# Performance work log

Measured on AMD Instinct MI355X. Metric: run time of the kernel, lower is better.

Reference implementation:

```python
import jax, jax.numpy as jnp
import numpy as np
from jax.experimental.ode import odeint

IN, H, OUT, NLAYERS = 256, 512, 128, 5
BATCH = 1024
RTOL, ATOL = 1e-7, 1e-9  # torchdiffeq dopri5 defaults


def _lin_init(key, fan_in, fan_out):
    kw, kb = jax.random.split(key)
    s = 1.0 / np.sqrt(fan_in)
    W = jax.random.uniform(kw, (fan_in, fan_out), jnp.float32, -s, s)
    b = jax.random.uniform(kb, (fan_out,), jnp.float32, -s, s)
    return W, b


def setup_inputs() -> dict:
    key = jax.random.key(0)
    ks = jax.random.split(key, 32)
    x = jax.random.normal(ks[0], (BATCH, IN), jnp.float32)
    Wi1, bi1 = _lin_init(ks[1], IN, H)
    Wi2, bi2 = _lin_init(ks[2], H, H)
    Wr, br = _lin_init(ks[3], IN, H)
    # 5 ODE funcs: Linear(H,2H) Tanh Linear(2H,2H) Tanh Linear(2H,H)
    oW1, ob1, oW2, ob2, oW3, ob3 = [], [], [], [], [], []
    for i in range(NLAYERS):
        a, b_ = _lin_init(ks[4 + 3 * i], H, 2 * H)
        c, d = _lin_init(ks[5 + 3 * i], 2 * H, 2 * H)
        e, f = _lin_init(ks[6 + 3 * i], 2 * H, H)
        oW1.append(a); ob1.append(b_); oW2.append(c); ob2.append(d); oW3.append(e); ob3.append(f)
    Wo1, bo1 = _lin_init(ks[20], H, H)
    Wo2, bo2 = _lin_init(ks[21], H, OUT)
    return {
        "x": x,
        "Wi1": Wi1, "bi1": bi1, "Wi2": Wi2, "bi2": bi2,
        "Wr": Wr, "br": br,
        "ode_W1": jnp.stack(oW1), "ode_b1": jnp.stack(ob1),
        "ode_W2": jnp.stack(oW2), "ode_b2": jnp.stack(ob2),
        "ode_W3": jnp.stack(oW3), "ode_b3": jnp.stack(ob3),
        "Wo1": Wo1, "bo1": bo1, "Wo2": Wo2, "bo2": bo2,
    }


def _forward(x, Wi1, bi1, Wi2, bi2, Wr, br,
             ode_W1, ode_b1, ode_W2, ode_b2, ode_W3, ode_b3,
             Wo1, bo1, Wo2, bo2):
    t = jnp.linspace(0.0, 1.0, 10)
    residual = x @ Wr + br                                  # [B, H]
    h = jnp.tanh(jnp.tanh(x @ Wi1 + bi1) @ Wi2 + bi2) + residual
    for i in range(NLAYERS):
        W1, b1 = ode_W1[i], ode_b1[i]
        W2, b2 = ode_W2[i], ode_b2[i]
        W3, b3 = ode_W3[i], ode_b3[i]

        def f(y, t_, W1=W1, b1=b1, W2=W2, b2=b2, W3=W3, b3=b3):
            return jnp.tanh(jnp.tanh(y @ W1 + b1) @ W2 + b2) @ W3 + b3

        h = odeint(f, h, t, rtol=RTOL, atol=ATOL)[-1]       # dopri5, take t=1
    return jnp.tanh(jnp.tanh(h @ Wo1 + bo1) @ Wo2 + bo2)   # [B, OUT]


def reference(x, Wi1, bi1, Wi2, bi2, Wr, br,
              ode_W1, ode_b1, ode_W2, ode_b2, ode_W3, ode_b3,
              Wo1, bo1, Wo2, bo2):
    return _forward(x, Wi1, bi1, Wi2, bi2, Wr, br,
                    ode_W1, ode_b1, ode_W2, ode_b2, ode_W3, ode_b3,
                    Wo1, bo1, Wo2, bo2)
```

## Files before the change

kernel.cpp:

```cpp
#include <hip/hip_runtime.h>
#include <hip/hip_bf16.h>
#include <math.h>

#define BATCH 1024
#define RKSTEPS 16

typedef __bf16 bf16x8 __attribute__((ext_vector_type(8)));
typedef float f32x16 __attribute__((ext_vector_type(16)));

enum { EM_PLAIN_F32=0, EM_TANH=1, EM_TANH_RES=2, EM_RK_FIRST=3, EM_RK_MID=4, EM_RK_LAST=5, EM_TANH_OUT=6 };

__device__ __forceinline__ unsigned short f2bf(float f){
    unsigned int u = __float_as_uint(f);
    u += 0x7fffu + ((u >> 16) & 1u);
    return (unsigned short)(u >> 16);
}
__device__ __forceinline__ float bf2f(unsigned short h){
    return __uint_as_float(((unsigned int)h) << 16);
}

__global__ __launch_bounds__(256) void xsplit(const float* __restrict__ src,
                                              unsigned short* __restrict__ h,
                                              unsigned short* __restrict__ l, int n){
    int i = blockIdx.x * 256 + threadIdx.x;
    if (i < n){
        float v = src[i];
        unsigned short hh = f2bf(v);
        h[i] = hh;
        l[i] = f2bf(v - bf2f(hh));
    }
}

__global__ __launch_bounds__(256) void wsplit_t(const float* __restrict__ W,
                                                unsigned short* __restrict__ Th,
                                                unsigned short* __restrict__ Tl,
                                                int K, int N){
    __shared__ float tile[32][33];
    const int k0 = blockIdx.x * 32;
    const int n0 = blockIdx.y * 32;
    const int t = threadIdx.x;
    const int r = t >> 3;
    const int c4 = (t & 7) * 4;
    const float4 v = *(const float4*)&W[(size_t)(k0 + r) * N + n0 + c4];
    tile[r][c4+0] = v.x; tile[r][c4+1] = v.y; tile[r][c4+2] = v.z; tile[r][c4+3] = v.w;
    __syncthreads();
    ushort4 hh, ll;
    #pragma unroll
    for (int j = 0; j < 4; ++j){
        float x = tile[c4 + j][r];
        unsigned short hb = f2bf(x);
        ((unsigned short*)&hh)[j] = hb;
        ((unsigned short*)&ll)[j] = f2bf(x - bf2f(hb));
    }
    *(ushort4*)&Th[(size_t)(n0 + r) * K + k0 + c4] = hh;
    *(ushort4*)&Tl[(size_t)(n0 + r) * K + k0 + c4] = ll;
}

__global__ __launch_bounds__(128) void gemm3p(
    const unsigned short* __restrict__ Ah, const unsigned short* __restrict__ Al,
    const unsigned short* __restrict__ Bh, const unsigned short* __restrict__ Bl,
    const float* __restrict__ bias,
    int M, int N, int K, int mode, float wk, float hc,
    unsigned short* __restrict__ outh, unsigned short* __restrict__ outl,
    float* outf, const float* res32, float* kacc32)
{
    __shared__ unsigned short Ash[32][72];
    __shared__ unsigned short Asl[32][72];
    __shared__ unsigned short Bsh[64][72];
    __shared__ unsigned short Bsl[64][72];

    const int tid  = threadIdx.x;
    const int lane = tid & 63;
    const int w    = tid >> 6;
    const int m0   = blockIdx.y * 32;
    const int n0   = blockIdx.x * 64;

    f32x16 accA, accB;
    #pragma unroll
    for (int i = 0; i < 16; ++i){ accA[i] = 0.f; accB[i] = 0.f; }

    uint4 rAh[2], rAl[2], rBh[4], rBl[4];

    auto stage_load = [&](int k0){
        #pragma unroll
        for (int p = 0; p < 2; ++p){
            int id = p * 128 + tid; int r = id >> 3; int c = (id & 7) * 8;
            size_t off = (size_t)(m0 + r) * K + k0 + c;
            rAh[p] = *(const uint4*)&Ah[off];
            rAl[p] = *(const uint4*)&Al[off];
        }
        #pragma unroll
        for (int p = 0; p < 4; ++p){
            int id = p * 128 + tid; int r = id >> 3; int c = (id & 7) * 8;
            size_t off = (size_t)(n0 + r) * K + k0 + c;
            rBh[p] = *(const uint4*)&Bh[off];
            rBl[p] = *(const uint4*)&Bl[off];
        }
    };
    auto stage_write = [&](){
        #pragma unroll
        for (int p = 0; p < 2; ++p){
            int id = p * 128 + tid; int r = id >> 3; int c = (id & 7) * 8;
            *(uint4*)&Ash[r][c] = rAh[p];
            *(uint4*)&Asl[r][c] = rAl[p];
        }
        #pragma unroll
        for (int p = 0; p < 4; ++p){
            int id = p * 128 + tid; int r = id >> 3; int c = (id & 7) * 8;
            *(uint4*)&Bsh[r][c] = rBh[p];
            *(uint4*)&Bsl[r][c] = rBl[p];
        }
    };

    stage_load(0);
    stage_write();
    __syncthreads();

    const int arow = lane & 31;
    const int brow = w * 32 + (lane & 31);
    const int g8   = (lane >> 5) * 8;

    for (int k0 = 0; k0 < K; k0 += 64){
        const bool more = (k0 + 64) < K;
        if (more) stage_load(k0 + 64);
        #pragma unroll
        for (int kc = 0; kc < 4; ++kc){
            const int koff = kc * 16 + g8;
            bf16x8 a_h = *(const bf16x8*)&Ash[arow][koff];
            bf16x8 a_l = *(const bf16x8*)&Asl[arow][koff];
            bf16x8 b_h = *(const bf16x8*)&Bsh[brow][koff];
            bf16x8 b_l = *(const bf16x8*)&Bsl[brow][koff];
            accA = __builtin_amdgcn_mfma_f32_32x32x16_bf16(a_h, b_h, accA, 0, 0, 0);
            accB = __builtin_amdgcn_mfma_f32_32x32x16_bf16(a_h, b_l, accB, 0, 0, 0);
            accB = __builtin_amdgcn_mfma_f32_32x32x16_bf16(a_l, b_h, accB, 0, 0, 0);
        }
        if (more){
            __syncthreads();
            stage_write();
            __syncthreads();
        }
    }

    const int col = n0 + w * 32 + (lane & 31);
    const float bc = bias[col];
    const int g4 = (lane >> 5) * 4;
    #pragma unroll
    for (int r = 0; r < 16; ++r){
        const int row = m0 + (r & 3) + 8 * (r >> 2) + g4;
        const size_t idx = (size_t)row * N + col;
        float z = accA[r] + accB[r] + bc;
        if (mode == EM_PLAIN_F32){
            outf[idx] = z;
        } else if (mode == EM_TANH){
            float t = tanhf(z);
            unsigned short hh = f2bf(t);
            outh[idx] = hh; outl[idx] = f2bf(t - bf2f(hh));
        } else if (mode == EM_TANH_RES){
            float t = tanhf(z) + res32[idx];
            outf[idx] = t;
            unsigned short hh = f2bf(t);
            outh[idx] = hh; outl[idx] = f2bf(t - bf2f(hh));
        } else if (mode == EM_RK_FIRST){
            kacc32[idx] = z;
            float yt = res32[idx] + hc * z;
            unsigned short hh = f2bf(yt);
            outh[idx] = hh; outl[idx] = f2bf(yt - bf2f(hh));
        } else if (mode == EM_RK_MID){
            kacc32[idx] += wk * z;
            float yt = res32[idx] + hc * z;
            unsigned short hh = f2bf(yt);
            outh[idx] = hh; outl[idx] = f2bf(yt - bf2f(hh));
        } else if (mode == EM_RK_LAST){
            float ynew = res32[idx] + hc * (kacc32[idx] + z);
            outf[idx] = ynew;
            unsigned short hh = f2bf(ynew);
            outh[idx] = hh; outl[idx] = f2bf(ynew - bf2f(hh));
        } else {
            outf[idx] = tanhf(z);
        }
    }
}

extern "C" void kernel_launch(void* const* d_in, const int* in_sizes, int n_in,
                              void* d_out, int out_size, void* d_ws, size_t ws_size,
                              hipStream_t stream)
{
    (void)in_sizes; (void)n_in; (void)out_size; (void)ws_size;
    const float* x   = (const float*)d_in[0];
    const float* Wi1 = (const float*)d_in[1];
    const float* bi1 = (const float*)d_in[2];
    const float* Wi2 = (const float*)d_in[3];
    const float* bi2 = (const float*)d_in[4];
    const float* Wr  = (const float*)d_in[5];
    const float* br  = (const float*)d_in[6];
    const float* oW1 = (const float*)d_in[7];
    const float* ob1 = (const float*)d_in[8];
    const float* oW2 = (const float*)d_in[9];
    const float* ob2 = (const float*)d_in[10];
    const float* oW3 = (const float*)d_in[11];
    const float* ob3 = (const float*)d_in[12];
    const float* Wo1 = (const float*)d_in[13];
    const float* bo1 = (const float*)d_in[14];
    const float* Wo2 = (const float*)d_in[15];
    const float* bo2 = (const float*)d_in[16];
    float* out = (float*)d_out;

    typedef unsigned short us;
    char* p = (char*)d_ws;
    auto alloc = [&](size_t bytes)->char*{ char* r = p; p += (bytes + 255) & ~(size_t)255; return r; };

    us* xh = (us*)alloc(1024*256*2);  us* xl = (us*)alloc(1024*256*2);
    us* Wi1th = (us*)alloc(512*256*2);  us* Wi1tl = (us*)alloc(512*256*2);
    us* Wi2th = (us*)alloc(512*512*2);  us* Wi2tl = (us*)alloc(512*512*2);
    us* Wrth  = (us*)alloc(512*256*2);  us* Wrtl  = (us*)alloc(512*256*2);
    us* oW1th = (us*)alloc(5ull*1024*512*2);  us* oW1tl = (us*)alloc(5ull*1024*512*2);
    us* oW2th = (us*)alloc(5ull*1024*1024*2); us* oW2tl = (us*)alloc(5ull*1024*1024*2);
    us* oW3th = (us*)alloc(5ull*512*1024*2);  us* oW3tl = (us*)alloc(5ull*512*1024*2);
    us* Wo1th = (us*)alloc(512*512*2);  us* Wo1tl = (us*)alloc(512*512*2);
    us* Wo2th = (us*)alloc(128*512*2);  us* Wo2tl = (us*)alloc(128*512*2);
    us* t1h = (us*)alloc(1024ull*1024*2); us* t1l = (us*)alloc(1024ull*1024*2);
    us* a2h = (us*)alloc(1024ull*1024*2); us* a2l = (us*)alloc(1024ull*1024*2);
    us* yh  = (us*)alloc(1024ull*512*2);  us* yl  = (us*)alloc(1024ull*512*2);
    us* yth = (us*)alloc(1024ull*512*2);  us* ytl = (us*)alloc(1024ull*512*2);
    float* y32  = (float*)alloc(1024ull*512*4);
    float* kacc = (float*)alloc(1024ull*512*4);
    float* rres = (float*)alloc(1024ull*512*4);

    hipLaunchKernelGGL(xsplit, dim3(1024), dim3(256), 0, stream, x, xh, xl, 1024*256);
    auto WS = [&](const float* W, us* th, us* tl, int K, int N){
        hipLaunchKernelGGL(wsplit_t, dim3(K/32, N/32), dim3(256), 0, stream, W, th, tl, K, N);
    };
    WS(Wi1, Wi1th, Wi1tl, 256, 512);
    WS(Wi2, Wi2th, Wi2tl, 512, 512);
    WS(Wr,  Wrth,  Wrtl,  256, 512);
    for (int L = 0; L < 5; ++L){
        WS(oW1 + (size_t)L*512*1024,  oW1th + (size_t)L*1024*512,  oW1tl + (size_t)L*1024*512,  512, 1024);
        WS(oW2 + (size_t)L*1024*1024, oW2th + (size_t)L*1024*1024, oW2tl + (size_t)L*1024*1024, 1024, 1024);
        WS(oW3 + (size_t)L*1024*512,  oW3th + (size_t)L*512*1024,  oW3tl + (size_t)L*512*1024,  1024, 512);
    }
    WS(Wo1, Wo1th, Wo1tl, 512, 512);
    WS(Wo2, Wo2th, Wo2tl, 512, 128);

    auto G = [&](const us* ah, const us* al, const us* bh, const us* bl,
                 const float* bias, int N, int K, int mode, float wkv, float hcv,
                 us* oh, us* ol, float* of, const float* rs, float* ka){
        dim3 grid(N/64, BATCH/32);
        hipLaunchKernelGGL(gemm3p, grid, dim3(128), 0, stream,
                           ah, al, bh, bl, bias, BATCH, N, K, mode, wkv, hcv, oh, ol, of, rs, ka);
    };

    G(xh, xl, Wrth, Wrtl, br, 512, 256, EM_PLAIN_F32, 0.f, 0.f, nullptr, nullptr, rres, nullptr, nullptr);
    G(xh, xl, Wi1th, Wi1tl, bi1, 512, 256, EM_TANH, 0.f, 0.f, t1h, t1l, nullptr, nullptr, nullptr);
    G(t1h, t1l, Wi2th, Wi2tl, bi2, 512, 512, EM_TANH_RES, 0.f, 0.f, yh, yl, y32, rres, nullptr);

    const float hs = 1.0f / (float)RKSTEPS;
    for (int L = 0; L < 5; ++L){
        const us* W1h = oW1th + (size_t)L*1024*512;  const us* W1l = oW1tl + (size_t)L*1024*512;
        const us* W2h = oW2th + (size_t)L*1024*1024; const us* W2l = oW2tl + (size_t)L*1024*1024;
        const us* W3h = oW3th + (size_t)L*512*1024;  const us* W3l = oW3tl + (size_t)L*512*1024;
        const float* b1 = ob1 + (size_t)L*1024;
        const float* b2 = ob2 + (size_t)L*1024;
        const float* b3 = ob3 + (size_t)L*512;
        for (int s = 0; s < RKSTEPS; ++s){
            G(yh, yl, W1h, W1l, b1, 1024, 512,  EM_TANH, 0.f, 0.f, t1h, t1l, nullptr, nullptr, nullptr);
            G(t1h, t1l, W2h, W2l, b2, 1024, 1024, EM_TANH, 0.f, 0.f, a2h, a2l, nullptr, nullptr, nullptr);
            G(a2h, a2l, W3h, W3l, b3, 512, 1024, EM_RK_FIRST, 0.f, 0.5f*hs, yth, ytl, nullptr, y32, kacc);
            G(yth, ytl, W1h, W1l, b1, 1024, 512,  EM_TANH, 0.f, 0.f, t1h, t1l, nullptr, nullptr, nullptr);
            G(t1h, t1l, W2h, W2l, b2, 1024, 1024, EM_TANH, 0.f, 0.f, a2h, a2l, nullptr, nullptr, nullptr);
            G(a2h, a2l, W3h, W3l, b3, 512, 1024, EM_RK_MID, 2.f, 0.5f*hs, yth, ytl, nullptr, y32, kacc);
            G(yth, ytl, W1h, W1l, b1, 1024, 512,  EM_TANH, 0.f, 0.f, t1h, t1l, nullptr, nullptr, nullptr);
            G(t1h, t1l, W2h, W2l, b2, 1024, 1024, EM_TANH, 0.f, 0.f, a2h, a2l, nullptr, nullptr, nullptr);
            G(a2h, a2l, W3h, W3l, b3, 512, 1024, EM_RK_MID, 2.f, hs, yth, ytl, nullptr, y32, kacc);
            G(yth, ytl, W1h, W1l, b1, 1024, 512,  EM_TANH, 0.f, 0.f, t1h, t1l, nullptr, nullptr, nullptr);
            G(t1h, t1l, W2h, W2l, b2, 1024, 1024, EM_TANH, 0.f, 0.f, a2h, a2l, nullptr, nullptr, nullptr);
            G(a2h, a2l, W3h, W3l, b3, 512, 1024, EM_RK_LAST, 1.f, hs/6.f, yh, yl, y32, y32, kacc);
        }
    }

    G(yh, yl, Wo1th, Wo1tl, bo1, 512, 512, EM_TANH, 0.f, 0.f, t1h, t1l, nullptr, nullptr, nullptr);
    G(t1h, t1l, Wo2th, Wo2tl, bo2, 128, 512, EM_TANH_OUT, 0.f, 0.f, nullptr, nullptr, out, nullptr, nullptr);
}
```

Measured before the change: 43.26 ms.

## Fuse ODE RK4 loop into persistent kernel with grid barriers

Replaces the 960 separate GEMM launches of the RK4 integration with one persistent kernel of 256 blocks that loops over layers, steps and stages. A software grid barrier built on an atomic counter separates the GEMM phases. All 22 weight-split launches are merged into one table-driven kernel. This removes per-launch overhead and tail gaps, but it relies on all 256 blocks being co-resident, uses a timeout break in the barrier, and the third GEMM leaves half of its waves idle.

```diff
diff --git a/kernel.cpp b/kernel.cpp
--- a/kernel.cpp
+++ b/kernel.cpp
@@ -4,70 +4,83 @@
 
 #define BATCH 1024
 #define RKSTEPS 16
-
+#define NBLK 256
+
+typedef unsigned short us;
 typedef __bf16 bf16x8 __attribute__((ext_vector_type(8)));
 typedef float f32x16 __attribute__((ext_vector_type(16)));
 
-enum { EM_PLAIN_F32=0, EM_TANH=1, EM_TANH_RES=2, EM_RK_FIRST=3, EM_RK_MID=4, EM_RK_LAST=5, EM_TANH_OUT=6 };
-
-__device__ __forceinline__ unsigned short f2bf(float f){
+enum { EM_PLAIN_F32=0, EM_TANH=1, EM_TANH_RES=2, EM_TANH_OUT=6 };
+
+__device__ __forceinline__ us f2bf(float f){
     unsigned int u = __float_as_uint(f);
     u += 0x7fffu + ((u >> 16) & 1u);
-    return (unsigned short)(u >> 16);
-}
-__device__ __forceinline__ float bf2f(unsigned short h){
+    return (us)(u >> 16);
+}
+__device__ __forceinline__ float bf2f(us h){
     return __uint_as_float(((unsigned int)h) << 16);
 }
+__device__ __forceinline__ void split_store(float v, us* ph, us* pl, size_t idx){
+    us hh = f2bf(v); ph[idx] = hh; pl[idx] = f2bf(v - bf2f(hh));
+}
 
 __global__ __launch_bounds__(256) void xsplit(const float* __restrict__ src,
-                                              unsigned short* __restrict__ h,
-                                              unsigned short* __restrict__ l, int n){
+                                              us* __restrict__ h, us* __restrict__ l,
+                                              int n, unsigned* ctr){
+    if (blockIdx.x == 0 && threadIdx.x == 0) *ctr = 0u;
     int i = blockIdx.x * 256 + threadIdx.x;
     if (i < n){
         float v = src[i];
-        unsigned short hh = f2bf(v);
+        us hh = f2bf(v);
         h[i] = hh;
         l[i] = f2bf(v - bf2f(hh));
     }
 }
 
-__global__ __launch_bounds__(256) void wsplit_t(const float* __restrict__ W,
-                                                unsigned short* __restrict__ Th,
-                                                unsigned short* __restrict__ Tl,
-                                                int K, int N){
+struct WsDesc { const float* src; us* h; us* l; int K; int N; int tile0; };
+struct WsTable { WsDesc d[22]; };
+
+__global__ __launch_bounds__(256) void wsplit_all(WsTable T){
     __shared__ float tile[32][33];
-    const int k0 = blockIdx.x * 32;
-    const int n0 = blockIdx.y * 32;
-    const int t = threadIdx.x;
-    const int r = t >> 3;
-    const int c4 = (t & 7) * 4;
-    const float4 v = *(const float4*)&W[(size_t)(k0 + r) * N + n0 + c4];
+    const int t = blockIdx.x;
+    int mi = 0;
+    #pragma unroll 1
+    for (int i = 1; i < 22; ++i) if (t >= T.d[i].tile0) mi = i;
+    const WsDesc dd = T.d[mi];
+    const int local = t - dd.tile0;
+    const int tilesx = dd.K >> 5;
+    const int k0 = (local % tilesx) * 32;
+    const int n0 = (local / tilesx) * 32;
+    const int tt = threadIdx.x;
+    const int r = tt >> 3;
+    const int c4 = (tt & 7) * 4;
+    const float4 v = *(const float4*)&dd.src[(size_t)(k0 + r) * dd.N + n0 + c4];
     tile[r][c4+0] = v.x; tile[r][c4+1] = v.y; tile[r][c4+2] = v.z; tile[r][c4+3] = v.w;
     __syncthreads();
     ushort4 hh, ll;
     #pragma unroll
     for (int j = 0; j < 4; ++j){
         float x = tile[c4 + j][r];
-        unsigned short hb = f2bf(x);
-        ((unsigned short*)&hh)[j] = hb;
-        ((unsigned short*)&ll)[j] = f2bf(x - bf2f(hb));
-    }
-    *(ushort4*)&Th[(size_t)(n0 + r) * K + k0 + c4] = hh;
-    *(ushort4*)&Tl[(size_t)(n0 + r) * K + k0 + c4] = ll;
+        us hb = f2bf(x);
+        ((us*)&hh)[j] = hb;
+        ((us*)&ll)[j] = f2bf(x - bf2f(hb));
+    }
+    *(ushort4*)&dd.h[(size_t)(n0 + r) * dd.K + k0 + c4] = hh;
+    *(ushort4*)&dd.l[(size_t)(n0 + r) * dd.K + k0 + c4] = ll;
 }
 
 __global__ __launch_bounds__(128) void gemm3p(
-    const unsigned short* __restrict__ Ah, const unsigned short* __restrict__ Al,
-    const unsigned short* __restrict__ Bh, const unsigned short* __restrict__ Bl,
+    const us* __restrict__ Ah, const us* __restrict__ Al,
+    const us* __restrict__ Bh, const us* __restrict__ Bl,
     const float* __restrict__ bias,
-    int M, int N, int K, int mode, float wk, float hc,
-    unsigned short* __restrict__ outh, unsigned short* __restrict__ outl,
-    float* outf, const float* res32, float* kacc32)
+    int M, int N, int K, int mode,
+    us* __restrict__ outh, us* __restrict__ outl,
+    float* outf, const float* res32)
 {
-    __shared__ unsigned short Ash[32][72];
-    __shared__ unsigned short Asl[32][72];
-    __shared__ unsigned short Bsh[64][72];
-    __shared__ unsigned short Bsl[64][72];
+    __shared__ us Ash[32][72];
+    __shared__ us Asl[32][72];
+    __shared__ us Bsh[64][72];
+    __shared__ us Bsl[64][72];
 
     const int tid  = threadIdx.x;
     const int lane = tid & 63;
@@ -80,7 +93,6 @@
     for (int i = 0; i < 16; ++i){ accA[i] = 0.f; accB[i] = 0.f; }
 
     uint4 rAh[2], rAl[2], rBh[4], rBl[4];
-
     auto stage_load = [&](int k0){
         #pragma unroll
         for (int p = 0; p < 2; ++p){
@@ -153,30 +165,247 @@
             outf[idx] = z;
         } else if (mode == EM_TANH){
             float t = tanhf(z);
-            unsigned short hh = f2bf(t);
-            outh[idx] = hh; outl[idx] = f2bf(t - bf2f(hh));
+            split_store(t, outh, outl, idx);
         } else if (mode == EM_TANH_RES){
             float t = tanhf(z) + res32[idx];
             outf[idx] = t;
-            unsigned short hh = f2bf(t);
-            outh[idx] = hh; outl[idx] = f2bf(t - bf2f(hh));
-        } else if (mode == EM_RK_FIRST){
-            kacc32[idx] = z;
-            float yt = res32[idx] + hc * z;
-            unsigned short hh = f2bf(yt);
-            outh[idx] = hh; outl[idx] = f2bf(yt - bf2f(hh));
-        } else if (mode == EM_RK_MID){
-            kacc32[idx] += wk * z;
-            float yt = res32[idx] + hc * z;
-            unsigned short hh = f2bf(yt);
-            outh[idx] = hh; outl[idx] = f2bf(yt - bf2f(hh));
-        } else if (mode == EM_RK_LAST){
-            float ynew = res32[idx] + hc * (kacc32[idx] + z);
-            outf[idx] = ynew;
-            unsigned short hh = f2bf(ynew);
-            outh[idx] = hh; outl[idx] = f2bf(ynew - bf2f(hh));
+            split_store(t, outh, outl, idx);
         } else {
             outf[idx] = tanhf(z);
+        }
+    }
+}
+
+__device__ __forceinline__ void grid_bar(unsigned* ctr, unsigned target){
+    __syncthreads();
+    if (threadIdx.x == 0){
+        __threadfence();
+        __hip_atomic_fetch_add(ctr, 1u, __ATOMIC_ACQ_REL, __HIP_MEMORY_SCOPE_AGENT);
+        long long t0 = (long long)__builtin_amdgcn_s_memrealtime();
+        while (__hip_atomic_load(ctr, __ATOMIC_ACQUIRE, __HIP_MEMORY_SCOPE_AGENT) < target){
+            __builtin_amdgcn_s_sleep(1);
+            if ((long long)__builtin_amdgcn_s_memrealtime() - t0 > 200000000LL) break;
+        }
+        __threadfence();
+    }
+    __syncthreads();
+}
+
+__global__ __launch_bounds__(256, 1) void fused_ode(
+    const us* __restrict__ W1t_h, const us* __restrict__ W1t_l, const float* __restrict__ B1,
+    const us* __restrict__ W2t_h, const us* __restrict__ W2t_l, const float* __restrict__ B2,
+    const us* __restrict__ W3t_h, const us* __restrict__ W3t_l, const float* __restrict__ B3,
+    us* __restrict__ yh,  us* __restrict__ yl,
+    us* __restrict__ yth, us* __restrict__ ytl,
+    us* __restrict__ a1h, us* __restrict__ a1l,
+    us* __restrict__ a2h, us* __restrict__ a2l,
+    float* __restrict__ y32, float* __restrict__ kacc,
+    unsigned* ctr)
+{
+    __shared__ us smem[18432];
+    us* Ash = smem;
+    us* Asl = smem + 4608;
+    us* Bsh = smem + 9216;
+    us* Bsl = smem + 13824;
+
+    const int tid  = threadIdx.x;
+    const int lane = tid & 63;
+    const int w    = tid >> 6;
+    const int bid  = blockIdx.x;
+    const int mrow = (bid & 7) * 2 + ((bid >> 3) & 1);
+    const int ncol = bid >> 4;
+    const int m0  = mrow * 64;
+    const int n0  = ncol * 64;
+    const int n0c = ncol * 32;
+    const float hs = 1.0f / (float)RKSTEPS;
+    unsigned epoch = 0;
+
+    auto gemm64 = [&](const us* Ahp, const us* Alp, int sA,
+                      const us* Bhp, const us* Blp, int K,
+                      f32x16& c0, f32x16& c1, f32x16& c2){
+        uint4 rAh[2], rAl[2], rBh[2], rBl[2];
+        auto ld = [&](int k0){
+            #pragma unroll
+            for (int p = 0; p < 2; ++p){
+                int id = p * 256 + tid; int rr = id >> 3; int cc = (id & 7) * 8;
+                rAh[p] = *(const uint4*)&Ahp[(size_t)rr * sA + k0 + cc];
+                rAl[p] = *(const uint4*)&Alp[(size_t)rr * sA + k0 + cc];
+                rBh[p] = *(const uint4*)&Bhp[(size_t)rr * K + k0 + cc];
+                rBl[p] = *(const uint4*)&Blp[(size_t)rr * K + k0 + cc];
+            }
+        };
+        auto wr = [&](){
+            #pragma unroll
+            for (int p = 0; p < 2; ++p){
+                int id = p * 256 + tid; int rr = id >> 3; int cc = (id & 7) * 8;
+                *(uint4*)&Ash[rr * 72 + cc] = rAh[p];
+                *(uint4*)&Asl[rr * 72 + cc] = rAl[p];
+                *(uint4*)&Bsh[rr * 72 + cc] = rBh[p];
+                *(uint4*)&Bsl[rr * 72 + cc] = rBl[p];
+            }
+        };
+        const int aoff = ((w >> 1) * 32 + (lane & 31)) * 72;
+        const int boff = ((w & 1)  * 32 + (lane & 31)) * 72;
+        const int g8   = (lane >> 5) * 8;
+        ld(0);
+        for (int k0 = 0; k0 < K; k0 += 64){
+            wr(); __syncthreads();
+            if (k0 + 64 < K) ld(k0 + 64);
+            #pragma unroll
+            for (int kc = 0; kc < 4; ++kc){
+                int ko = kc * 16 + g8;
+                bf16x8 ah = *(const bf16x8*)&Ash[aoff + ko];
+                bf16x8 al = *(const bf16x8*)&Asl[aoff + ko];
+                bf16x8 bh = *(const bf16x8*)&Bsh[boff + ko];
+                bf16x8 bl = *(const bf16x8*)&Bsl[boff + ko];
+                c0 = __builtin_amdgcn_mfma_f32_32x32x16_bf16(ah, bh, c0, 0, 0, 0);
+                c1 = __builtin_amdgcn_mfma_f32_32x32x16_bf16(ah, bl, c1, 0, 0, 0);
+                c2 = __builtin_amdgcn_mfma_f32_32x32x16_bf16(al, bh, c2, 0, 0, 0);
+            }
+            __syncthreads();
+        }
+    };
+
+    auto gemmC = [&](const us* Ahp, const us* Alp,
+                     const us* Bhp, const us* Blp,
+                     f32x16& c0, f32x16& c1, f32x16& c2){
+        uint4 rAh[2], rAl[2], rBh, rBl;
+        auto ld = [&](int k0){
+            #pragma unroll
+            for (int p = 0; p < 2; ++p){
+                int id = p * 256 + tid; int rr = id >> 3; int cc = (id & 7) * 8;
+                rAh[p] = *(const uint4*)&Ahp[(size_t)rr * 1024 + k0 + cc];
+                rAl[p] = *(const uint4*)&Alp[(size_t)rr * 1024 + k0 + cc];
+            }
+            { int rr = tid >> 3; int cc = (tid & 7) * 8;
+              rBh = *(const uint4*)&Bhp[(size_t)rr * 1024 + k0 + cc];
+              rBl = *(const uint4*)&Blp[(size_t)rr * 1024 + k0 + cc]; }
+        };
+        auto wr = [&](){
+            #pragma unroll
+            for (int p = 0; p < 2; ++p){
+                int id = p * 256 + tid; int rr = id >> 3; int cc = (id & 7) * 8;
+                *(uint4*)&Ash[rr * 72 + cc] = rAh[p];
+                *(uint4*)&Asl[rr * 72 + cc] = rAl[p];
+            }
+            { int rr = tid >> 3; int cc = (tid & 7) * 8;
+              *(uint4*)&Bsh[rr * 72 + cc] = rBh;
+              *(uint4*)&Bsl[rr * 72 + cc] = rBl; }
+        };
+        const int aoff = ((w & 1) * 32 + (lane & 31)) * 72;
+        const int boff = (lane & 31) * 72;
+        const int g8   = (lane >> 5) * 8;
+        ld(0);
+        for (int k0 = 0; k0 < 1024; k0 += 64){
+            wr(); __syncthreads();
+            if (k0 + 64 < 1024) ld(k0 + 64);
+            if (w < 2){
+                #pragma unroll
+                for (int kc = 0; kc < 4; ++kc){
+                    int ko = kc * 16 + g8;
+                    bf16x8 ah = *(const bf16x8*)&Ash[aoff + ko];
+                    bf16x8 al = *(const bf16x8*)&Asl[aoff + ko];
+                    bf16x8 bh = *(const bf16x8*)&Bsh[boff + ko];
+                    bf16x8 bl = *(const bf16x8*)&Bsl[boff + ko];
+                    c0 = __builtin_amdgcn_mfma_f32_32x32x16_bf16(ah, bh, c0, 0, 0, 0);
+                    c1 = __builtin_amdgcn_mfma_f32_32x32x16_bf16(ah, bl, c1, 0, 0, 0);
+                    c2 = __builtin_amdgcn_mfma_f32_32x32x16_bf16(al, bh, c2, 0, 0, 0);
+                }
+            }
+            __syncthreads();
+        }
+    };
+
+    #pragma unroll 1
+    for (int L = 0; L < 5; ++L){
+        const us* W1h = W1t_h + (size_t)L * 1024 * 512;
+        const us* W1l = W1t_l + (size_t)L * 1024 * 512;
+        const us* W2h = W2t_h + (size_t)L * 1024 * 1024;
+        const us* W2l = W2t_l + (size_t)L * 1024 * 1024;
+        const us* W3h = W3t_h + (size_t)L * 512 * 1024;
+        const us* W3l = W3t_l + (size_t)L * 512 * 1024;
+        const float* b1 = B1 + L * 1024;
+        const float* b2 = B2 + L * 1024;
+        const float* b3 = B3 + L * 512;
+
+        #pragma unroll 1
+        for (int st = 0; st < RKSTEPS; ++st){
+            #pragma unroll 1
+            for (int s = 0; s < 4; ++s){
+                const us* inh = (s == 0) ? yh : yth;
+                const us* inl = (s == 0) ? yl : ytl;
+
+                {
+                    f32x16 c0, c1, c2;
+                    #pragma unroll
+                    for (int i = 0; i < 16; ++i){ c0[i]=0.f; c1[i]=0.f; c2[i]=0.f; }
+                    gemm64(inh + (size_t)m0 * 512, inl + (size_t)m0 * 512, 512,
+                           W1h + (size_t)n0 * 512, W1l + (size_t)n0 * 512, 512,
+                           c0, c1, c2);
+                    const int col = n0 + (w & 1) * 32 + (lane & 31);
+                    const float bb = b1[col];
+                    const int rbase = m0 + (w >> 1) * 32 + 4 * (lane >> 5);
+                    #pragma unroll
+                    for (int r = 0; r < 16; ++r){
+                        int row = rbase + (r & 3) + 8 * (r >> 2);
+                        float z = c0[r] + c1[r] + c2[r] + bb;
+                        split_store(tanhf(z), a1h, a1l, (size_t)row * 1024 + col);
+                    }
+                }
+                ++epoch; grid_bar(ctr, epoch * NBLK);
+
+                {
+                    f32x16 c0, c1, c2;
+                    #pragma unroll
+                    for (int i = 0; i < 16; ++i){ c0[i]=0.f; c1[i]=0.f; c2[i]=0.f; }
+                    gemm64(a1h + (size_t)m0 * 1024, a1l + (size_t)m0 * 1024, 1024,
+                           W2h + (size_t)n0 * 1024, W2l + (size_t)n0 * 1024, 1024,
+                           c0, c1, c2);
+                    const int col = n0 + (w & 1) * 32 + (lane & 31);
+                    const float bb = b2[col];
+                    const int rbase = m0 + (w >> 1) * 32 + 4 * (lane >> 5);
+                    #pragma unroll
+                    for (int r = 0; r < 16; ++r){
+                        int row = rbase + (r & 3) + 8 * (r >> 2);
+                        float z = c0[r] + c1[r] + c2[r] + bb;
+                        split_store(tanhf(z), a2h, a2l, (size_t)row * 1024 + col);
+                    }
+                }
+                ++epoch; grid_bar(ctr, epoch * NBLK);
+
+                {
+                    f32x16 c0, c1, c2;
+                    #pragma unroll
+                    for (int i = 0; i < 16; ++i){ c0[i]=0.f; c1[i]=0.f; c2[i]=0.f; }
+                    gemmC(a2h + (size_t)m0 * 1024, a2l + (size_t)m0 * 1024,
+                          W3h + (size_t)n0c * 1024, W3l + (size_t)n0c * 1024,
+                          c0, c1, c2);
+                    if (w < 2){
+                        const int col = n0c + (lane & 31);
+                        const float bb = b3[col];
+                        const int rbase = m0 + (w & 1) * 32 + 4 * (lane >> 5);
+                        #pragma unroll
+                        for (int r = 0; r < 16; ++r){
+                            int row = rbase + (r & 3) + 8 * (r >> 2);
+                            size_t idx = (size_t)row * 512 + col;
+                            float z = c0[r] + c1[r] + c2[r] + bb;
+                            if (s == 0){
+                                kacc[idx] = z;
+                                split_store(y32[idx] + 0.5f * hs * z, yth, ytl, idx);
+                            } else if (s == 3){
+                                float yn = y32[idx] + (hs / 6.0f) * (kacc[idx] + z);
+                                y32[idx] = yn;
+                                split_store(yn, yh, yl, idx);
+                            } else {
+                                kacc[idx] += 2.0f * z;
+                                float hc = (s == 1) ? 0.5f * hs : hs;
+                                split_store(y32[idx] + hc * z, yth, ytl, idx);
+                            }
+                        }
+                    }
+                }
+                ++epoch; grid_bar(ctr, epoch * NBLK);
+            }
         }
     }
 }
@@ -205,7 +434,6 @@
     const float* bo2 = (const float*)d_in[16];
     float* out = (float*)d_out;
 
-    typedef unsigned short us;
     char* p = (char*)d_ws;
     auto alloc = [&](size_t bytes)->char*{ char* r = p; p += (bytes + 255) & ~(size_t)255; return r; };
 
@@ -218,65 +446,57 @@
     us* oW3th = (us*)alloc(5ull*512*1024*2);  us* oW3tl = (us*)alloc(5ull*512*1024*2);
     us* Wo1th = (us*)alloc(512*512*2);  us* Wo1tl = (us*)alloc(512*512*2);
     us* Wo2th = (us*)alloc(128*512*2);  us* Wo2tl = (us*)alloc(128*512*2);
-    us* t1h = (us*)alloc(1024ull*1024*2); us* t1l = (us*)alloc(1024ull*1024*2);
+    us* t1h = (us*)alloc(1024ull*512*2);  us* t1l = (us*)alloc(1024ull*512*2);
+    us* a1h = (us*)alloc(1024ull*1024*2); us* a1l = (us*)alloc(1024ull*1024*2);
     us* a2h = (us*)alloc(1024ull*1024*2); us* a2l = (us*)alloc(1024ull*1024*2);
     us* yh  = (us*)alloc(1024ull*512*2);  us* yl  = (us*)alloc(1024ull*512*2);
     us* yth = (us*)alloc(1024ull*512*2);  us* ytl = (us*)alloc(1024ull*512*2);
     float* y32  = (float*)alloc(1024ull*512*4);
     float* kacc = (float*)alloc(1024ull*512*4);
-    float* rres = (float*)alloc(1024ull*512*4);
-
-    hipLaunchKernelGGL(xsplit, dim3(1024), dim3(256), 0, stream, x, xh, xl, 1024*256);
-    auto WS = [&](const float* W, us* th, us* tl, int K, int N){
-        hipLaunchKernelGGL(wsplit_t, dim3(K/32, N/32), dim3(256), 0, stream, W, th, tl, K, N);
+    unsigned* ctr = (unsigned*)alloc(256);
+    float* rres = kacc;
+
+    hipLaunchKernelGGL(xsplit, dim3(1024), dim3(256), 0, stream, x, xh, xl, 1024*256, ctr);
+
+    WsTable T;
+    for (int i = 0; i < 22; ++i){
+        T.d[i].src = nullptr; T.d[i].h = nullptr; T.d[i].l = nullptr;
+        T.d[i].K = 32; T.d[i].N = 32; T.d[i].tile0 = 0x7fffffff;
+    }
+    int tile_acc = 0, di = 0;
+    auto addW = [&](const float* W, us* th, us* tl, int K, int N){
+        T.d[di].src = W; T.d[di].h = th; T.d[di].l = tl;
+        T.d[di].K = K; T.d[di].N = N; T.d[di].tile0 = tile_acc;
+        tile_acc += (K/32) * (N/32); ++di;
     };
-    WS(Wi1, Wi1th, Wi1tl, 256, 512);
-    WS(Wi2, Wi2th, Wi2tl, 512, 512);
-    WS(Wr,  Wrth,  Wrtl,  256, 512);
+    addW(Wi1, Wi1th, Wi1tl, 256, 512);
+    addW(Wi2, Wi2th, Wi2tl, 512, 512);
+    addW(Wr,  Wrth,  Wrtl,  256, 512);
     for (int L = 0; L < 5; ++L){
-        WS(oW1 + (size_t)L*512*1024,  oW1th + (size_t)L*1024*512,  oW1tl + (size_t)L*1024*512,  512, 1024);
-        WS(oW2 + (size_t)L*1024*1024, oW2th + (size_t)L*1024*1024, oW2tl + (size_t)L*1024*1024, 1024, 1024);
-        WS(oW3 + (size_t)L*1024*512,  oW3th + (size_t)L*512*1024,  oW3tl + (size_t)L*512*1024,  1024, 512);
-    }
-    WS(Wo1, Wo1th, Wo1tl, 512, 512);
-    WS(Wo2, Wo2th, Wo2tl, 512, 128);
+        addW(oW1 + (size_t)L*512*1024,  oW1th + (size_t)L*1024*512,  oW1tl + (size_t)L*1024*512,  512, 1024);
+        addW(oW2 + (size_t)L*1024*1024, oW2th + (size_t)L*1024*1024, oW2tl + (size_t)L*1024*1024, 1024, 1024);
+        addW(oW3 + (size_t)L*1024*512,  oW3th + (size_t)L*512*1024,  oW3tl + (size_t)L*512*1024,  1024, 512);
+    }
+    addW(Wo1, Wo1th, Wo1tl, 512, 512);
+    addW(Wo2, Wo2th, Wo2tl, 512, 128);
+    hipLaunchKernelGGL(wsplit_all, dim3(tile_acc), dim3(256), 0, stream, T);
 
     auto G = [&](const us* ah, const us* al, const us* bh, const us* bl,
-                 const float* bias, int N, int K, int mode, float wkv, float hcv,
-                 us* oh, us* ol, float* of, const float* rs, float* ka){
+                 const float* bias, int N, int K, int mode,
+                 us* oh, us* ol, float* of, const float* rs){
         dim3 grid(N/64, BATCH/32);
         hipLaunchKernelGGL(gemm3p, grid, dim3(128), 0, stream,
-                           ah, al, bh, bl, bias, BATCH, N, K, mode, wkv, hcv, oh, ol, of, rs, ka);
+                           ah, al, bh, bl, bias, BATCH, N, K, mode, oh, ol, of, rs);
     };
 
-    G(xh, xl, Wrth, Wrtl, br, 512, 256, EM_PLAIN_F32, 0.f, 0.f, nullptr, nullptr, rres, nullptr, nullptr);
-    G(xh, xl, Wi1th, Wi1tl, bi1, 512, 256, EM_TANH, 0.f, 0.f, t1h, t1l, nullptr, nullptr, nullptr);
-    G(t1h, t1l, Wi2th, Wi2tl, bi2, 512, 512, EM_TANH_RES, 0.f, 0.f, yh, yl, y32, rres, nullptr);
-
-    const float hs = 1.0f / (float)RKSTEPS;
-    for (int L = 0; L < 5; ++L){
-        const us* W1h = oW1th + (size_t)L*1024*512;  const us* W1l = oW1tl + (size_t)L*1024*512;
-        const us* W2h = oW2th + (size_t)L*1024*1024; const us* W2l = oW2tl + (size_t)L*1024*1024;
-        const us* W3h = oW3th + (size_t)L*512*1024;  const us* W3l = oW3tl + (size_t)L*512*1024;
-        const float* b1 = ob1 + (size_t)L*1024;
-        const float* b2 = ob2 + (size_t)L*1024;
-        const float* b3 = ob3 + (size_t)L*512;
-        for (int s = 0; s < RKSTEPS; ++s){
-            G(yh, yl, W1h, W1l, b1, 1024, 512,  EM_TANH, 0.f, 0.f, t1h, t1l, nullptr, nullptr, nullptr);
-            G(t1h, t1l, W2h, W2l, b2, 1024, 1024, EM_TANH, 0.f, 0.f, a2h, a2l, nullptr, nullptr, nullptr);
-            G(a2h, a2l, W3h, W3l, b3, 512, 1024, EM_RK_FIRST, 0.f, 0.5f*hs, yth, ytl, nullptr, y32, kacc);
-            G(yth, ytl, W1h, W1l, b1, 1024, 512,  EM_TANH, 0.f, 0.f, t1h, t1l, nullptr, nullptr, nullptr);
-            G(t1h, t1l, W2h, W2l, b2, 1024, 1024, EM_TANH, 0.f, 0.f, a2h, a2l, nullptr, nullptr, nullptr);
-            G(a2h, a2l, W3h, W3l, b3, 512, 1024, EM_RK_MID, 2.f, 0.5f*hs, yth, ytl, nullptr, y32, kacc);
-            G(yth, ytl, W1h, W1l, b1, 1024, 512,  EM_TANH, 0.f, 0.f, t1h, t1l, nullptr, nullptr, nullptr);
-            G(t1h, t1l, W2h, W2l, b2, 1024, 1024, EM_TANH, 0.f, 0.f, a2h, a2l, nullptr, nullptr, nullptr);
-            G(a2h, a2l, W3h, W3l, b3, 512, 1024, EM_RK_MID, 2.f, hs, yth, ytl, nullptr, y32, kacc);
-            G(yth, ytl, W1h, W1l, b1, 1024, 512,  EM_TANH, 0.f, 0.f, t1h, t1l, nullptr, nullptr, nullptr);
-            G(t1h, t1l, W2h, W2l, b2, 1024, 1024, EM_TANH, 0.f, 0.f, a2h, a2l, nullptr, nullptr, nullptr);
-            G(a2h, a2l, W3h, W3l, b3, 512, 1024, EM_RK_LAST, 1.f, hs/6.f, yh, yl, y32, y32, kacc);
-        }
-    }
-
-    G(yh, yl, Wo1th, Wo1tl, bo1, 512, 512, EM_TANH, 0.f, 0.f, t1h, t1l, nullptr, nullptr, nullptr);
-    G(t1h, t1l, Wo2th, Wo2tl, bo2, 128, 512, EM_TANH_OUT, 0.f, 0.f, nullptr, nullptr, out, nullptr, nullptr);
-}
+    G(xh, xl, Wrth, Wrtl, br, 512, 256, EM_PLAIN_F32, nullptr, nullptr, rres, nullptr);
+    G(xh, xl, Wi1th, Wi1tl, bi1, 512, 256, EM_TANH, t1h, t1l, nullptr, nullptr);
+    G(t1h, t1l, Wi2th, Wi2tl, bi2, 512, 512, EM_TANH_RES, yh, yl, y32, rres);
+
+    hipLaunchKernelGGL(fused_ode, dim3(NBLK), dim3(256), 0, stream,
+                       oW1th, oW1tl, ob1, oW2th, oW2tl, ob2, oW3th, oW3tl, ob3,
+                       yh, yl, yth, ytl, a1h, a1l, a2h, a2l, y32, kacc, ctr);
+
+    G(yh, yl, Wo1th, Wo1tl, bo1, 512, 512, EM_TANH, t1h, t1l, nullptr, nullptr);
+    G(t1h, t1l, Wo2th, Wo2tl, bo2, 128, 512, EM_TANH_OUT, nullptr, nullptr, out, nullptr);
+}
```

Measured after the change: 66.80 ms. 54.4% more time.
